# Optimization experiments

Measured on AMD Instinct MI355X. Metric: run time of the kernel, lower is better.

Reference implementation:

```python
import jax, jax.numpy as jnp
import numpy as np
from jax import lax

BN_EPS = 1e-5


def setup_inputs() -> dict:
    key = jax.random.key(0)
    ks = jax.random.split(key, 3)
    B, N, D = 96, 20, 2048
    return {
        "x": jax.random.normal(ks[0], (B, N, D), dtype=jnp.float32),
        "conv_w": jax.random.normal(ks[1], (D, 2 * D), dtype=jnp.float32) * 0.02,
        "conv_b": jax.random.normal(ks[2], (D,), dtype=jnp.float32) * 0.02,
        "bn_gamma": jnp.ones((D,), dtype=jnp.float32),
        "bn_beta": jnp.zeros((D,), dtype=jnp.float32),
        "bn_mean": jnp.zeros((D,), dtype=jnp.float32),
        "bn_var": jnp.ones((D,), dtype=jnp.float32),
        "n_neighbor": 10,
    }


def reference(x, conv_w, conv_b, bn_gamma, bn_beta, bn_mean, bn_var, n_neighbor):
    # x: [B, N, D] -> xt: [B, D, N] (channels-first point cloud of view features)
    xt = jnp.transpose(x, (0, 2, 1))
    B, D, N = xt.shape
    k = int(n_neighbor)

    # pairwise squared distances: [B, N, N]
    sq = jnp.sum(xt * xt, axis=1, keepdims=True)            # [B, 1, N]
    inner = jnp.einsum("bdn,bdm->bnm", xt, xt)              # [B, N, N]
    adj = sq + (-2.0) * inner + jnp.transpose(sq, (0, 2, 1))

    # k nearest neighbors (smallest distance) -> idx [B, N, k]
    _, nn_idx = lax.top_k(-adj, k)

    # gather neighbor features without the O(N^2) expand: [B, D, N, k]
    neighbors = jax.vmap(lambda xb, idx: xb[:, idx])(xt, nn_idx)

    center = xt[:, :, :, None]                              # [B, D, N, 1]
    edge = jnp.concatenate(
        [jnp.broadcast_to(center, (B, D, N, k)), neighbors - center], axis=1
    )                                                       # [B, 2D, N, k]

    # 1x1 conv (GEMM over channel dim) + BatchNorm (inference) + ReLU
    y = jnp.einsum("oc,bcnk->bonk", conv_w, edge) + conv_b[None, :, None, None]
    inv = bn_gamma / jnp.sqrt(bn_var + BN_EPS)
    y = y * inv[None, :, None, None] + (bn_beta - bn_mean * inv)[None, :, None, None]
    y = jax.nn.relu(y)

    # max over neighbors, then max over points -> [B, D, 1, 1]
    y = jnp.max(y, axis=-1, keepdims=True)
    y = jnp.max(y, axis=2, keepdims=True)
    return y
```

## Files before the change

### kernel.cpp

```cpp
#include <hip/hip_runtime.h>
#include <hip/hip_bf16.h>
#include <math.h>

#define BN_EPS 1e-5f
#define B_  96
#define N_  20
#define D_  2048
#define K_  10
#define M_  (B_*N_)
#define R_  (2*D_)

typedef __attribute__((ext_vector_type(8))) short bf16x8;
typedef __attribute__((ext_vector_type(4))) float f32x4;
typedef __attribute__((ext_vector_type(8))) unsigned short ushort8;

static __device__ __forceinline__ unsigned short f2bf(float f) {
  unsigned int u = __builtin_bit_cast(unsigned int, f);
  u = u + 0x7fffu + ((u >> 16) & 1u);
  return (unsigned short)(u >> 16);
}

#define GLOAD_LDS16(g, l) \
  __builtin_amdgcn_global_load_lds((const __attribute__((address_space(1))) void*)(g), \
                                   (__attribute__((address_space(3))) void*)(l), 16, 0, 0)

__global__ __launch_bounds__(512) void gram_kernel(const float* __restrict__ x,
                                                   float* __restrict__ innr_g)
{
  int t = threadIdx.x, w = t >> 6, lane = t & 63;
  int task = blockIdx.x * 8 + w;
  int b = task / N_, n = task % N_;
  const float* xb = x + (size_t)b * N_ * D_;
  const float4* pn = (const float4*)(xb + n * D_);
  float4 c[8];
  #pragma unroll
  for (int j = 0; j < 8; ++j) c[j] = pn[lane + 64*j];
  float* ig = innr_g + b * (N_*N_);
  for (int m = n; m < N_; ++m) {
    const float4* pm = (const float4*)(xb + m * D_);
    float s0 = 0.f, s1 = 0.f, s2 = 0.f, s3 = 0.f;
    #pragma unroll
    for (int j = 0; j < 8; ++j) {
      float4 v = pm[lane + 64*j];
      float d = fmaf(c[j].x, v.x, fmaf(c[j].y, v.y,
                fmaf(c[j].z, v.z, c[j].w * v.w)));
      if      ((j&3)==0) s0 += d;
      else if ((j&3)==1) s1 += d;
      else if ((j&3)==2) s2 += d;
      else               s3 += d;
    }
    float s = (s0 + s1) + (s2 + s3);
    #pragma unroll
    for (int off = 32; off > 0; off >>= 1)
      s += __shfl_xor(s, off, 64);
    if (lane == 0) { ig[n*N_ + m] = s; ig[m*N_ + n] = s; }
  }
}

__global__ __launch_bounds__(64) void topk_kernel(const float* __restrict__ innr_g,
                                                  int* __restrict__ nn_idx)
{
  int b = blockIdx.x, t = threadIdx.x;
  __shared__ float adjl[N_*N_];
  const float* ig = innr_g + b * (N_*N_);
  for (int p = t; p < N_*N_; p += 64) {
    int n = p / N_, m = p % N_;
    adjl[p] = ig[n*N_+n] + ig[m*N_+m] - 2.f * ig[p];
  }
  __syncthreads();
  if (t < N_) {
    int n = t;
    unsigned mask = 0;
    for (int it = 0; it < K_; ++it) {
      float bv = INFINITY; int bi = 0;
      for (int m = 0; m < N_; ++m) {
        if (!((mask >> m) & 1u)) {
          float v = adjl[n*N_+m];
          if (v < bv) { bv = v; bi = m; }
        }
      }
      mask |= 1u << bi;
      nn_idx[(b*N_ + n)*K_ + it] = bi;
    }
  }
}

__global__ __launch_bounds__(512) void cast_kernel(const float* __restrict__ x,
                                                   const float* __restrict__ cw,
                                                   unsigned short* __restrict__ Xb,
                                                   unsigned short* __restrict__ Wn)
{
  int q = blockIdx.x * 512 + threadIdx.x;
  const float* sp[4];
  ushort8* dp[4];
  #pragma unroll
  for (int s = 0; s < 4; ++s) {
    int i = q + s * 385024;
    if (i < 491520) {
      sp[s] = x + (size_t)i * 8;
      dp[s] = (ushort8*)Xb + i;
    } else {
      int j = i - 491520;
      int r = j >> 8, k = (j & 255) * 8;
      sp[s] = cw + (size_t)(r >> 1) * R_ + ((r & 1) << 11) + k;
      dp[s] = (ushort8*)Wn + j;
    }
  }
  float4 a[4], c[4];
  #pragma unroll
  for (int s = 0; s < 4; ++s) { a[s] = *(const float4*)sp[s]; c[s] = *(const float4*)(sp[s] + 4); }
  #pragma unroll
  for (int s = 0; s < 4; ++s) {
    ushort8 o = { f2bf(a[s].x), f2bf(a[s].y), f2bf(a[s].z), f2bf(a[s].w),
                  f2bf(c[s].x), f2bf(c[s].y), f2bf(c[s].z), f2bf(c[s].w) };
    *dp[s] = o;
  }
}

__global__ __launch_bounds__(256, 3) void fused_gemm(
    const unsigned short* __restrict__ Xb, const unsigned short* __restrict__ Wn,
    const int* __restrict__ nn_idx, const float* __restrict__ conv_b,
    const float* __restrict__ gamma, const float* __restrict__ beta,
    const float* __restrict__ mean, const float* __restrict__ var,
    float* __restrict__ out)
{
  __shared__ __align__(16) char smem[53248];
  float* Cl  = (float*)smem;
  int*   idxl = (int*)(smem + 40960);

  int flat = blockIdx.y * 24 + blockIdx.x;
  int nf = (flat & 7) * 96 + (flat >> 3);
  int bx = nf % 24, by = nf / 24;

  int t = threadIdx.x, lane = t & 63, w = t >> 6;
  int m0 = bx * 80, b0 = bx * 4;
  int r0 = by * 128, o0 = by * 64;
  int rowsel = lane & 15, ksel = lane >> 4;

  f32x4 acc[5][2] = {};

  auto stage = [&](int sel, int k0) {
    unsigned short* Asb = (unsigned short*)(smem + sel*26624);
    unsigned short* Bsb = (unsigned short*)(smem + sel*26624 + 10240);
    #pragma unroll
    for (int i = 0; i < 3; ++i) {
      int fl = i*256 + t;
      if (fl < 640) {
        int row = fl >> 3, kc = fl & 7;
        GLOAD_LDS16(Xb + (size_t)(m0 + row) * D_ + k0 + ((kc ^ (row & 7)) << 3),
                    Asb + fl*8);
      }
    }
    #pragma unroll
    for (int i = 0; i < 4; ++i) {
      int fl = i*256 + t;
      int row = fl >> 3, kc = fl & 7;
      GLOAD_LDS16(Wn + (size_t)(r0 + row) * D_ + k0 + ((kc ^ (row & 7)) << 3),
                  Bsb + fl*8);
    }
  };

  auto compute = [&](int sel) {
    unsigned short* Asb = (unsigned short*)(smem + sel*26624);
    unsigned short* Bsb = (unsigned short*)(smem + sel*26624 + 10240);
    #pragma unroll
    for (int ks = 0; ks < 2; ++ks) {
      int swz = ((ks*4 + ksel) ^ (rowsel & 7)) << 3;
      bf16x8 a[5], bfr[2];
      #pragma unroll
      for (int mi = 0; mi < 5; ++mi)
        a[mi] = *(const bf16x8*)(Asb + (mi*16 + rowsel)*64 + swz);
      #pragma unroll
      for (int ri = 0; ri < 2; ++ri)
        bfr[ri] = *(const bf16x8*)(Bsb + (w*32 + ri*16 + rowsel)*64 + swz);
      #pragma unroll
      for (int mi = 0; mi < 5; ++mi)
        #pragma unroll
        for (int ri = 0; ri < 2; ++ri)
          acc[mi][ri] = __builtin_amdgcn_mfma_f32_16x16x32_bf16(a[mi], bfr[ri], acc[mi][ri], 0, 0, 0);
    }
  };

  stage(0, 0);
  for (int kt = 0; kt < D_/64; ++kt) {
    __syncthreads();
    if (kt + 1 < D_/64) stage((kt+1) & 1, (kt+1)*64);
    compute(kt & 1);
  }
  __syncthreads();

  #pragma unroll
  for (int mi = 0; mi < 5; ++mi)
    #pragma unroll
    for (int ri = 0; ri < 2; ++ri)
      #pragma unroll
      for (int rg = 0; rg < 4; ++rg)
        Cl[(mi*16 + ksel*4 + rg)*128 + w*32 + ri*16 + rowsel] = acc[mi][ri][rg];
  for (int i = t; i < 4*N_*K_; i += 256) idxl[i] = nn_idx[b0*N_*K_ + i];
  __syncthreads();

  int bb = w, oo = lane;
  int og = o0 + oo;
  float invv  = gamma[og] / sqrtf(var[og] + BN_EPS);
  float shift = fmaf(-mean[og], invv, beta[og]);
  float bias  = conv_b[og];
  float best = 0.f;
  int rbase = bb * N_;
  for (int n = 0; n < N_; ++n) {
    float Pv = Cl[(rbase + n)*128 + oo*2];
    float Qn = Cl[(rbase + n)*128 + oo*2 + 1];
    float aa = Pv - Qn + bias;
    const int* ix = idxl + bb*N_*K_ + n*K_;
    #pragma unroll
    for (int kk = 0; kk < K_; ++kk) {
      int j = ix[kk];
      float v = fmaf(aa + Cl[(rbase + j)*128 + oo*2 + 1], invv, shift);
      best = fmaxf(best, v);
    }
  }
  out[(size_t)(b0 + bb) * D_ + og] = best;
}

extern "C" void kernel_launch(void* const* d_in, const int* in_sizes, int n_in,
                              void* d_out, int out_size, void* d_ws, size_t ws_size,
                              hipStream_t stream)
{
  const float* x      = (const float*)d_in[0];
  const float* conv_w = (const float*)d_in[1];
  const float* conv_b = (const float*)d_in[2];
  const float* gamma  = (const float*)d_in[3];
  const float* beta   = (const float*)d_in[4];
  const float* mean   = (const float*)d_in[5];
  const float* var    = (const float*)d_in[6];

  int* nn_idx = (int*)d_ws;
  unsigned short* Xb = (unsigned short*)((char*)d_ws + 76800);
  unsigned short* Wn = (unsigned short*)((char*)d_ws + 76800 + (size_t)M_*D_*2);
  float* innr_g = (float*)((char*)d_ws + 76800 + (size_t)M_*D_*2 + (size_t)R_*D_*2);

  gram_kernel<<<240, 512, 0, stream>>>(x, innr_g);
  topk_kernel<<<B_, 64, 0, stream>>>(innr_g, nn_idx);
  cast_kernel<<<752, 512, 0, stream>>>(x, conv_w, Xb, Wn);
  fused_gemm<<<dim3(24, 32), 256, 0, stream>>>(
      Xb, Wn, nn_idx, conv_b, gamma, beta, mean, var, (float*)d_out);
}
```

Before: 92.40 us.

## Merge gram, cast and top-k into prep kernel and GEMM epilogue

The gram, cast and top-k kernels are replaced by a single prep kernel. Its first 240 blocks compute the Gram matrix and cast x to bf16, and the remaining blocks cast the conv weights. The top-k neighbor selection moves into the fused GEMM epilogue, which rebuilds the distance matrix in LDS for its 4 batches from the Gram output. This cuts the launch count from four to two and drops the nn_idx round trip. In exchange, every GEMM block redundantly recomputes top-k for its batches, with 80 threads running a serial selection loop while the rest wait.

```diff
diff --git a/kernel.cpp b/kernel.cpp
--- a/kernel.cpp
+++ b/kernel.cpp
@@ -24,10 +24,35 @@
   __builtin_amdgcn_global_load_lds((const __attribute__((address_space(1))) void*)(g), \
                                    (__attribute__((address_space(3))) void*)(l), 16, 0, 0)
 
-__global__ __launch_bounds__(512) void gram_kernel(const float* __restrict__ x,
-                                                   float* __restrict__ innr_g)
+__global__ __launch_bounds__(512) void prep_kernel(const float* __restrict__ x,
+                                                   const float* __restrict__ cw,
+                                                   float* __restrict__ innr_g,
+                                                   unsigned short* __restrict__ Xb,
+                                                   unsigned short* __restrict__ Wn)
 {
-  int t = threadIdx.x, w = t >> 6, lane = t & 63;
+  int t = threadIdx.x;
+  if (blockIdx.x >= 240) {
+    int q = (blockIdx.x - 240) * 512 + t;
+    const float* sp[4]; ushort8* dp[4];
+    #pragma unroll
+    for (int s = 0; s < 4; ++s) {
+      int j = q + s * 262144;
+      int r = j >> 8, k = (j & 255) * 8;
+      sp[s] = cw + (size_t)(r >> 1) * R_ + ((r & 1) << 11) + k;
+      dp[s] = (ushort8*)Wn + j;
+    }
+    float4 a[4], c[4];
+    #pragma unroll
+    for (int s = 0; s < 4; ++s) { a[s] = *(const float4*)sp[s]; c[s] = *(const float4*)(sp[s] + 4); }
+    #pragma unroll
+    for (int s = 0; s < 4; ++s) {
+      ushort8 o = { f2bf(a[s].x), f2bf(a[s].y), f2bf(a[s].z), f2bf(a[s].w),
+                    f2bf(c[s].x), f2bf(c[s].y), f2bf(c[s].z), f2bf(c[s].w) };
+      *dp[s] = o;
+    }
+    return;
+  }
+  int w = t >> 6, lane = t & 63;
   int task = blockIdx.x * 8 + w;
   int b = task / N_, n = task % N_;
   const float* xb = x + (size_t)b * N_ * D_;
@@ -55,78 +80,39 @@
       s += __shfl_xor(s, off, 64);
     if (lane == 0) { ig[n*N_ + m] = s; ig[m*N_ + n] = s; }
   }
-}
-
-__global__ __launch_bounds__(64) void topk_kernel(const float* __restrict__ innr_g,
-                                                  int* __restrict__ nn_idx)
-{
-  int b = blockIdx.x, t = threadIdx.x;
-  __shared__ float adjl[N_*N_];
-  const float* ig = innr_g + b * (N_*N_);
-  for (int p = t; p < N_*N_; p += 64) {
-    int n = p / N_, m = p % N_;
-    adjl[p] = ig[n*N_+n] + ig[m*N_+m] - 2.f * ig[p];
-  }
-  __syncthreads();
-  if (t < N_) {
-    int n = t;
-    unsigned mask = 0;
-    for (int it = 0; it < K_; ++it) {
-      float bv = INFINITY; int bi = 0;
-      for (int m = 0; m < N_; ++m) {
-        if (!((mask >> m) & 1u)) {
-          float v = adjl[n*N_+m];
-          if (v < bv) { bv = v; bi = m; }
-        }
-      }
-      mask |= 1u << bi;
-      nn_idx[(b*N_ + n)*K_ + it] = bi;
-    }
-  }
-}
-
-__global__ __launch_bounds__(512) void cast_kernel(const float* __restrict__ x,
-                                                   const float* __restrict__ cw,
-                                                   unsigned short* __restrict__ Xb,
-                                                   unsigned short* __restrict__ Wn)
-{
-  int q = blockIdx.x * 512 + threadIdx.x;
-  const float* sp[4];
-  ushort8* dp[4];
-  #pragma unroll
-  for (int s = 0; s < 4; ++s) {
-    int i = q + s * 385024;
-    if (i < 491520) {
+  {
+    int q = blockIdx.x * 2048 + t;
+    const float* sp[4]; ushort8* dp[4];
+    #pragma unroll
+    for (int s = 0; s < 4; ++s) {
+      int i = q + s * 512;
       sp[s] = x + (size_t)i * 8;
       dp[s] = (ushort8*)Xb + i;
-    } else {
-      int j = i - 491520;
-      int r = j >> 8, k = (j & 255) * 8;
-      sp[s] = cw + (size_t)(r >> 1) * R_ + ((r & 1) << 11) + k;
-      dp[s] = (ushort8*)Wn + j;
-    }
-  }
-  float4 a[4], c[4];
-  #pragma unroll
-  for (int s = 0; s < 4; ++s) { a[s] = *(const float4*)sp[s]; c[s] = *(const float4*)(sp[s] + 4); }
-  #pragma unroll
-  for (int s = 0; s < 4; ++s) {
-    ushort8 o = { f2bf(a[s].x), f2bf(a[s].y), f2bf(a[s].z), f2bf(a[s].w),
-                  f2bf(c[s].x), f2bf(c[s].y), f2bf(c[s].z), f2bf(c[s].w) };
-    *dp[s] = o;
+    }
+    float4 a[4], cc[4];
+    #pragma unroll
+    for (int s = 0; s < 4; ++s) { a[s] = *(const float4*)sp[s]; cc[s] = *(const float4*)(sp[s] + 4); }
+    #pragma unroll
+    for (int s = 0; s < 4; ++s) {
+      ushort8 o = { f2bf(a[s].x), f2bf(a[s].y), f2bf(a[s].z), f2bf(a[s].w),
+                    f2bf(cc[s].x), f2bf(cc[s].y), f2bf(cc[s].z), f2bf(cc[s].w) };
+      *dp[s] = o;
+    }
   }
 }
 
 __global__ __launch_bounds__(256, 3) void fused_gemm(
     const unsigned short* __restrict__ Xb, const unsigned short* __restrict__ Wn,
-    const int* __restrict__ nn_idx, const float* __restrict__ conv_b,
+    const float* __restrict__ innr_g, const float* __restrict__ conv_b,
     const float* __restrict__ gamma, const float* __restrict__ beta,
     const float* __restrict__ mean, const float* __restrict__ var,
     float* __restrict__ out)
 {
   __shared__ __align__(16) char smem[53248];
-  float* Cl  = (float*)smem;
+  float* Cl   = (float*)smem;
   int*   idxl = (int*)(smem + 40960);
+  float* adjt = (float*)(smem + 44160);
+  float* dl   = (float*)(smem + 50560);
 
   int flat = blockIdx.y * 24 + blockIdx.x;
   int nf = (flat & 7) * 96 + (flat >> 3);
@@ -196,7 +182,32 @@
       #pragma unroll
       for (int rg = 0; rg < 4; ++rg)
         Cl[(mi*16 + ksel*4 + rg)*128 + w*32 + ri*16 + rowsel] = acc[mi][ri][rg];
-  for (int i = t; i < 4*N_*K_; i += 256) idxl[i] = nn_idx[b0*N_*K_ + i];
+  for (int i = t; i < 4*N_*N_; i += 256) adjt[i] = innr_g[b0*N_*N_ + i];
+  if (t < 4*N_) dl[t] = innr_g[(b0 + t/N_)*N_*N_ + (t%N_)*(N_+1)];
+  __syncthreads();
+
+  for (int i = t; i < 4*N_*N_; i += 256) {
+    int bb = i / (N_*N_), p = i % (N_*N_);
+    adjt[i] = dl[bb*N_ + p/N_] + dl[bb*N_ + p%N_] - 2.f * adjt[i];
+  }
+  __syncthreads();
+
+  if (t < 4*N_) {
+    int bb = t / N_, n = t % N_;
+    const float* row = adjt + bb*N_*N_ + n*N_;
+    unsigned mask = 0;
+    for (int it = 0; it < K_; ++it) {
+      float bv = INFINITY; int bi = 0;
+      for (int m = 0; m < N_; ++m) {
+        if (!((mask >> m) & 1u)) {
+          float v = row[m];
+          if (v < bv) { bv = v; bi = m; }
+        }
+      }
+      mask |= 1u << bi;
+      idxl[(bb*N_ + n)*K_ + it] = bi;
+    }
+  }
   __syncthreads();
 
   int bb = w, oo = lane;
@@ -233,14 +244,11 @@
   const float* mean   = (const float*)d_in[5];
   const float* var    = (const float*)d_in[6];
 
-  int* nn_idx = (int*)d_ws;
   unsigned short* Xb = (unsigned short*)((char*)d_ws + 76800);
   unsigned short* Wn = (unsigned short*)((char*)d_ws + 76800 + (size_t)M_*D_*2);
   float* innr_g = (float*)((char*)d_ws + 76800 + (size_t)M_*D_*2 + (size_t)R_*D_*2);
 
-  gram_kernel<<<240, 512, 0, stream>>>(x, innr_g);
-  topk_kernel<<<B_, 64, 0, stream>>>(innr_g, nn_idx);
-  cast_kernel<<<752, 512, 0, stream>>>(x, conv_w, Xb, Wn);
+  prep_kernel<<<752, 512, 0, stream>>>(x, conv_w, innr_g, Xb, Wn);
   fused_gemm<<<dim3(24, 32), 256, 0, stream>>>(
-      Xb, Wn, nn_idx, conv_b, gamma, beta, mean, var, (float*)d_out);
-}
+      Xb, Wn, innr_g, conv_b, gamma, beta, mean, var, (float*)d_out);
+}
```

Result: slower. 95.82 us (+3.7%).
